# Optimization experiments

Measured on AMD Instinct MI355X. Metric: run time of the kernel, lower is better.

The kernel has to match this reference:

```python
import jax, jax.numpy as jnp
import numpy as np


def setup_inputs() -> dict:
    key = jax.random.key(0)
    k1, k2, k3, k4 = jax.random.split(key, 4)
    B, N, IN_DIM, QK_DIM = 8, 2048, 10, 32
    s = jax.random.normal(k1, (B, N, IN_DIM), dtype=jnp.float32)
    G = jax.random.uniform(k2, (B, N, N), dtype=jnp.float32)
    Wq = jax.random.normal(k3, (QK_DIM, IN_DIM), dtype=jnp.float32) * (1.0 / np.sqrt(IN_DIM))
    Wk = jax.random.normal(k4, (QK_DIM, IN_DIM), dtype=jnp.float32) * (1.0 / np.sqrt(IN_DIM))
    return {"s": s, "G": G, "Wq": Wq, "Wk": Wk}


def reference(s, G, Wq, Wk):
    # q, k: [B, N, qk_dim]  (nn.Linear with no bias: x @ W^T)
    q = jnp.einsum("bnd,qd->bnq", s, Wq)
    k = jnp.einsum("bnd,qd->bnq", s, Wk)
    # logits: [B, N, N]
    logits = jnp.einsum("bnq,bmq->bnm", q, k)
    w = jnp.square(logits) * G
    w = w / (jnp.sum(w, axis=-1, keepdims=True) + 1e-06)
    return w
```

## Files before the change

kernel.cpp:

```cpp
#include <hip/hip_runtime.h>
#include <stdint.h>

#define BB 8
#define NN 2048
#define IND 10
#define QK 32

typedef float f32x4 __attribute__((ext_vector_type(4)));

__global__ __launch_bounds__(256) void qk_kernel(
    const float* __restrict__ s,
    const float* __restrict__ Wq, const float* __restrict__ Wk,
    float* __restrict__ q_ws, float* __restrict__ kt_ws) {
  int t = blockIdx.x * 256 + threadIdx.x;
  int b  = t >> 16;
  int n  = (t >> 5) & (NN - 1);
  int qd = t & 31;
  const float* srow = s + (size_t)(b * NN + n) * IND;
  float acq = 0.f, ack = 0.f;
#pragma unroll
  for (int d = 0; d < IND; ++d) {
    float sv = srow[d];
    acq = fmaf(sv, Wq[qd * IND + d], acq);
    ack = fmaf(sv, Wk[qd * IND + d], ack);
  }
  q_ws[(size_t)(b * NN + n) * QK + qd] = acq;
  int w  = n >> 9;
  int m  = n & 511;
  int i  = (m & 255) >> 2;
  int jc = ((m < 256) ? 0 : 4) + (m & 3);
  int ev = qd >> 2, c = qd & 3;
  kt_ws[(((size_t)(b * 4 + w) * 4096) + (ev * 8 + jc) * 64 + i) * 4 + c] = ack;
}

__global__ __launch_bounds__(256) void attn_kernel(
    const float* __restrict__ G,
    const float* __restrict__ q_ws, const float* __restrict__ kt_ws,
    float* __restrict__ out) {
  const int tid = threadIdx.x;
  const int b = blockIdx.y;
  const int r0 = blockIdx.x * 8;
  const int w = tid >> 6, lane = tid & 63;

  __shared__ float q_lds[4][256];
  __shared__ float red[4][8];

  {
    const float* qb = q_ws + ((size_t)b * NN + r0) * QK;
    *(float4*)&q_lds[w][4 * lane] = *(const float4*)&qb[4 * lane];
  }

  float acc[8][8];
#pragma unroll
  for (int r = 0; r < 8; ++r)
#pragma unroll
    for (int j = 0; j < 8; ++j) acc[r][j] = 0.f;

  const float4* kt =
      (const float4*)kt_ws + (size_t)(b * 4 + w) * 4096 + lane;

  float4 ka[8], kb[8];
#pragma unroll
  for (int j = 0; j < 8; ++j) ka[j] = kt[j * 64];

#pragma unroll
  for (int ev = 0; ev < 8; ++ev) {
    if (ev < 7) {
#pragma unroll
      for (int j = 0; j < 8; ++j) kb[j] = kt[((ev + 1) * 8 + j) * 64];
    }
#pragma unroll
    for (int r = 0; r < 8; ++r) {
      float q4[4];
      *(float4*)q4 = *(const float4*)&q_lds[w][r * 32 + ev * 4];
#pragma unroll
      for (int j = 0; j < 8; ++j) {
        acc[r][j] = fmaf(q4[0], ka[j].x, acc[r][j]);
        acc[r][j] = fmaf(q4[1], ka[j].y, acc[r][j]);
        acc[r][j] = fmaf(q4[2], ka[j].z, acc[r][j]);
        acc[r][j] = fmaf(q4[3], ka[j].w, acc[r][j]);
      }
    }
#pragma unroll
    for (int j = 0; j < 8; ++j) ka[j] = kb[j];
  }

  const float* gb = G + ((size_t)b * NN + r0) * NN + 512 * w + 4 * lane;
  float rsum[8];
#pragma unroll
  for (int r = 0; r < 8; ++r) {
    float gg[8];
    *(float4*)&gg[0] = *(const float4*)(gb + (size_t)r * NN);
    *(float4*)&gg[4] = *(const float4*)(gb + (size_t)r * NN + 256);
    float sum = 0.f;
#pragma unroll
    for (int j = 0; j < 8; ++j) {
      float v = acc[r][j];
      v = v * v * gg[j];
      acc[r][j] = v;
      sum += v;
    }
#pragma unroll
    for (int off = 32; off >= 1; off >>= 1) sum += __shfl_xor(sum, off, 64);
    rsum[r] = sum;
  }

  if ((tid & 63) == 0) {
#pragma unroll
    for (int r = 0; r < 8; ++r) red[w][r] = rsum[r];
  }
  __syncthreads();

  float inv[8];
#pragma unroll
  for (int r = 0; r < 8; ++r) {
    float total = red[0][r] + red[1][r] + red[2][r] + red[3][r];
    inv[r] = 1.0f / (total + 1e-6f);
  }

  float* ob = out + ((size_t)b * NN + r0) * NN + 512 * w + 4 * lane;
#pragma unroll
  for (int r = 0; r < 8; ++r) {
    f32x4 o0, o1;
    o0.x = acc[r][0] * inv[r]; o0.y = acc[r][1] * inv[r];
    o0.z = acc[r][2] * inv[r]; o0.w = acc[r][3] * inv[r];
    o1.x = acc[r][4] * inv[r]; o1.y = acc[r][5] * inv[r];
    o1.z = acc[r][6] * inv[r]; o1.w = acc[r][7] * inv[r];
    __builtin_nontemporal_store(o0, (f32x4*)(ob + (size_t)r * NN));
    __builtin_nontemporal_store(o1, (f32x4*)(ob + (size_t)r * NN + 256));
  }
}

extern "C" void kernel_launch(void* const* d_in, const int* in_sizes, int n_in,
                              void* d_out, int out_size, void* d_ws, size_t ws_size,
                              hipStream_t stream) {
  const float* s  = (const float*)d_in[0];
  const float* G  = (const float*)d_in[1];
  const float* Wq = (const float*)d_in[2];
  const float* Wk = (const float*)d_in[3];
  float* out = (float*)d_out;

  float* q_ws  = (float*)d_ws;
  float* kt_ws = q_ws + (size_t)BB * NN * QK;

  qk_kernel<<<(BB * NN * QK) / 256, 256, 0, stream>>>(s, Wq, Wk, q_ws, kt_ws);

  dim3 grid(NN / 8, BB);
  attn_kernel<<<grid, 256, 0, stream>>>(G, q_ws, kt_ws, out);
}
```

Measured before the change: 64.67 us.

## Split attention columns across eight waves and hoist G row loads

Result: slower. 73.90 us (+14.3%).

```diff
diff --git a/kernel.cpp b/kernel.cpp
--- a/kernel.cpp
+++ b/kernel.cpp
@@ -25,15 +25,14 @@
     ack = fmaf(sv, Wk[qd * IND + d], ack);
   }
   q_ws[(size_t)(b * NN + n) * QK + qd] = acq;
-  int w  = n >> 9;
-  int m  = n & 511;
-  int i  = (m & 255) >> 2;
-  int jc = ((m < 256) ? 0 : 4) + (m & 3);
+  int w  = n >> 8;
+  int i  = (n >> 2) & 63;
+  int j  = n & 3;
   int ev = qd >> 2, c = qd & 3;
-  kt_ws[(((size_t)(b * 4 + w) * 4096) + (ev * 8 + jc) * 64 + i) * 4 + c] = ack;
+  kt_ws[((((size_t)(b * 8 + w) * 8) + ev) * 256 + j * 64 + i) * 4 + c] = ack;
 }
 
-__global__ __launch_bounds__(256) void attn_kernel(
+__global__ __launch_bounds__(512) void attn_kernel(
     const float* __restrict__ G,
     const float* __restrict__ q_ws, const float* __restrict__ kt_ws,
     float* __restrict__ out) {
@@ -42,39 +41,39 @@
   const int r0 = blockIdx.x * 8;
   const int w = tid >> 6, lane = tid & 63;
 
-  __shared__ float q_lds[4][256];
-  __shared__ float red[4][8];
+  __shared__ float q_lds[8][256];
+  __shared__ float red[8][8];
 
   {
     const float* qb = q_ws + ((size_t)b * NN + r0) * QK;
     *(float4*)&q_lds[w][4 * lane] = *(const float4*)&qb[4 * lane];
   }
 
-  float acc[8][8];
+  float acc[8][4];
 #pragma unroll
   for (int r = 0; r < 8; ++r)
 #pragma unroll
-    for (int j = 0; j < 8; ++j) acc[r][j] = 0.f;
+    for (int j = 0; j < 4; ++j) acc[r][j] = 0.f;
 
   const float4* kt =
-      (const float4*)kt_ws + (size_t)(b * 4 + w) * 4096 + lane;
+      (const float4*)kt_ws + (size_t)(b * 8 + w) * 2048 + lane;
 
-  float4 ka[8], kb[8];
+  float4 ka[4], kb[4];
 #pragma unroll
-  for (int j = 0; j < 8; ++j) ka[j] = kt[j * 64];
+  for (int j = 0; j < 4; ++j) ka[j] = kt[j * 64];
 
 #pragma unroll
   for (int ev = 0; ev < 8; ++ev) {
     if (ev < 7) {
 #pragma unroll
-      for (int j = 0; j < 8; ++j) kb[j] = kt[((ev + 1) * 8 + j) * 64];
+      for (int j = 0; j < 4; ++j) kb[j] = kt[(ev + 1) * 256 + j * 64];
     }
 #pragma unroll
     for (int r = 0; r < 8; ++r) {
       float q4[4];
       *(float4*)q4 = *(const float4*)&q_lds[w][r * 32 + ev * 4];
 #pragma unroll
-      for (int j = 0; j < 8; ++j) {
+      for (int j = 0; j < 4; ++j) {
         acc[r][j] = fmaf(q4[0], ka[j].x, acc[r][j]);
         acc[r][j] = fmaf(q4[1], ka[j].y, acc[r][j]);
         acc[r][j] = fmaf(q4[2], ka[j].z, acc[r][j]);
@@ -82,19 +81,23 @@
       }
     }
 #pragma unroll
-    for (int j = 0; j < 8; ++j) ka[j] = kb[j];
+    for (int j = 0; j < 4; ++j) ka[j] = kb[j];
   }
 
-  const float* gb = G + ((size_t)b * NN + r0) * NN + 512 * w + 4 * lane;
+  const float* gb = G + ((size_t)b * NN + r0) * NN + 256 * w + 4 * lane;
+  float4 g0[8];
+#pragma unroll
+  for (int r = 0; r < 8; ++r) g0[r] = *(const float4*)(gb + (size_t)r * NN);
+  __builtin_amdgcn_sched_barrier(0);
+
   float rsum[8];
 #pragma unroll
   for (int r = 0; r < 8; ++r) {
-    float gg[8];
-    *(float4*)&gg[0] = *(const float4*)(gb + (size_t)r * NN);
-    *(float4*)&gg[4] = *(const float4*)(gb + (size_t)r * NN + 256);
+    float gg[4];
+    *(float4*)&gg[0] = g0[r];
     float sum = 0.f;
 #pragma unroll
-    for (int j = 0; j < 8; ++j) {
+    for (int j = 0; j < 4; ++j) {
       float v = acc[r][j];
       v = v * v * gg[j];
       acc[r][j] = v;
@@ -114,20 +117,21 @@
   float inv[8];
 #pragma unroll
   for (int r = 0; r < 8; ++r) {
-    float total = red[0][r] + red[1][r] + red[2][r] + red[3][r];
+    float total = 0.f;
+#pragma unroll
+    for (int w2 = 0; w2 < 8; ++w2) total += red[w2][r];
     inv[r] = 1.0f / (total + 1e-6f);
   }
 
-  float* ob = out + ((size_t)b * NN + r0) * NN + 512 * w + 4 * lane;
+  float* ob = out + ((size_t)b * NN + r0) * NN + 256 * w + 4 * lane;
 #pragma unroll
   for (int r = 0; r < 8; ++r) {
-    f32x4 o0, o1;
-    o0.x = acc[r][0] * inv[r]; o0.y = acc[r][1] * inv[r];
-    o0.z = acc[r][2] * inv[r]; o0.w = acc[r][3] * inv[r];
-    o1.x = acc[r][4] * inv[r]; o1.y = acc[r][5] * inv[r];
-    o1.z = acc[r][6] * inv[r]; o1.w = acc[r][7] * inv[r];
-    __builtin_nontemporal_store(o0, (f32x4*)(ob + (size_t)r * NN));
-    __builtin_nontemporal_store(o1, (f32x4*)(ob + (size_t)r * NN + 256));
+    f32x4 o;
+    o.x = acc[r][0] * inv[r];
+    o.y = acc[r][1] * inv[r];
+    o.z = acc[r][2] * inv[r];
+    o.w = acc[r][3] * inv[r];
+    __builtin_nontemporal_store(o, (f32x4*)(ob + (size_t)r * NN));
   }
 }
 
@@ -146,5 +150,5 @@
   qk_kernel<<<(BB * NN * QK) / 256, 256, 0, stream>>>(s, Wq, Wk, q_ws, kt_ws);
 
   dim3 grid(NN / 8, BB);
-  attn_kernel<<<grid, 256, 0, stream>>>(G, q_ws, kt_ws, out);
+  attn_kernel<<<grid, 512, 0, stream>>>(G, q_ws, kt_ws, out);
 }
```
